# Kernel tuning notes

Hardware: AMD Instinct MI355X
Metric: run time of the kernel (lower is better)

The kernel has to match this reference:

```python
import jax, jax.numpy as jnp
import numpy as np

B, S, H, I = 2, 2048, 4096, 14336

def setup_inputs() -> dict:
    key = jax.random.key(0)
    k1, k2, k3, k4 = jax.random.split(key, 4)
    sH = 1.0 / np.sqrt(H)
    sI = 1.0 / np.sqrt(I)
    return {
        "x": jax.random.normal(k1, (B, S, H), dtype=jnp.float32),
        "w_gate": jax.random.normal(k2, (I, H), dtype=jnp.float32) * sH,
        "w_up": jax.random.normal(k3, (I, H), dtype=jnp.float32) * sH,
        "w_down": jax.random.normal(k4, (H, I), dtype=jnp.float32) * sI,
    }

def reference(x, w_gate, w_up, w_down):
    # SwiGLU gated MLP: down( silu(x @ Wg^T) * (x @ Wu^T) )
    g = jnp.einsum("bsh,ih->bsi", x, w_gate)   # [B,S,I]
    u = jnp.einsum("bsh,ih->bsi", x, w_up)     # [B,S,I]
    a = jax.nn.silu(g) * u                      # fused silu_mul
    d = jnp.einsum("bsi,hi->bsh", a, w_down)   # [B,S,H]
    return d
```

## Files before the change

kernel.cpp:

```cpp
#include <hip/hip_runtime.h>
#include <hip/hip_bf16.h>
#include <stdint.h>

typedef __bf16 bf16_t;
typedef __bf16 bf16x4 __attribute__((ext_vector_type(4)));
typedef __bf16 bf16x8 __attribute__((ext_vector_type(8)));
typedef float f32x4 __attribute__((ext_vector_type(4)));

#define LDS_CAST(p) ((__attribute__((address_space(3))) void*)(p))
#define GLB_CAST(p) ((const __attribute__((address_space(1))) void*)(p))

__device__ __forceinline__ void gl_lds16(const void* g, void* l) {
  __builtin_amdgcn_global_load_lds(GLB_CAST(g), LDS_CAST(l), 16, 0, 0);
}

#define MFMA16(a,b,c) __builtin_amdgcn_mfma_f32_16x16x32_bf16((a),(b),(c),0,0,0)
#define BARRIER() __builtin_amdgcn_s_barrier()
#define LGKM0()  asm volatile("s_waitcnt lgkmcnt(0)" ::: "memory")
#define PRIO(n)  __builtin_amdgcn_s_setprio(n)

template<int N> __device__ __forceinline__ void vmw() {
  if constexpr (N == 8)      asm volatile("s_waitcnt vmcnt(8)" ::: "memory");
  else if constexpr (N == 4) asm volatile("s_waitcnt vmcnt(4)" ::: "memory");
  else if constexpr (N == 0) asm volatile("s_waitcnt vmcnt(0)" ::: "memory");
}

static constexpr int M_TOT = 4096, H_DIM = 4096, I_DIM = 14336;

__global__ __launch_bounds__(256)
void k_conv(const float4* __restrict__ src, bf16x4* __restrict__ dst, long n4)
{
  long stride = (long)gridDim.x * blockDim.x;
  for (long i = (long)blockIdx.x * blockDim.x + threadIdx.x; i < n4; i += stride) {
    float4 v = src[i];
    bf16x4 o;
    o[0] = (bf16_t)v.x; o[1] = (bf16_t)v.y; o[2] = (bf16_t)v.z; o[3] = (bf16_t)v.w;
    dst[i] = o;
  }
}

__global__ __launch_bounds__(512, 2)
void k_gateup9(const bf16_t* __restrict__ X, const bf16_t* __restrict__ Wg,
               const bf16_t* __restrict__ Wu, bf16_t* __restrict__ Aout)
{
  __shared__ __align__(1024) char lds[131072];
  const int tid = threadIdx.x, wave = tid >> 6, lane = tid & 63;
  const int lr = lane & 15, kg = lane >> 4;
  const int xm = ((lr >> 3) & 1) << 5;
  const int wm = wave >> 2, wn = wave & 3;
  const int wb = wave * 1024;

  const int bid = blockIdx.x;
  const int bq  = bid >> 3;
  const int tn  = (bid & 7) * 14 + (bq >> 4);
  const int tm  = bq & 15;

  const int srow  = tid >> 2;
  const int scolb = ((tid & 3) * 16) ^ (((tid >> 5) & 1) << 5);

  const bf16_t* gX = X  + (size_t)(tm * 256 + srow) * H_DIM + (scolb >> 1);
  const bf16_t* gG = Wg + (size_t)(tn * 128 + srow) * H_DIM + (scolb >> 1);
  const bf16_t* gU = Wu + (size_t)(tn * 128 + srow) * H_DIM + (scolb >> 1);
  const size_t xh = (size_t)128 * H_DIM;

  const int ck   = (kg * 16) ^ xm;
  const int offA = (wm * 128 + lr) * 64 + ck;
  const int offG = 16384 + (wn * 32 + lr) * 64 + ck;
  const int offU = offG + 8192;

  const f32x4 vz = {0.f, 0.f, 0.f, 0.f};
  f32x4 accg[8][2], accu[8][2];
#pragma unroll
  for (int m = 0; m < 8; ++m)
#pragma unroll
    for (int n = 0; n < 2; ++n) { accg[m][n] = vz; accu[m][n] = vz; }

#define G1_STAGE(TT)                                                         \
  { char* sb = lds + (((TT) & 3) << 15) + wb;                                \
    const int kc = (TT) * 32;                                                \
    gl_lds16(gX + kc,      sb);                                              \
    gl_lds16(gX + xh + kc, sb + 8192);                                       \
    gl_lds16(gG + kc,      sb + 16384);                                      \
    gl_lds16(gU + kc,      sb + 24576); }

#define G1_READS(SET, TT)                                                    \
  { const char* rb = lds + (((TT) & 3) << 15);                               \
    _Pragma("unroll") for (int f = 0; f < 8; ++f)                            \
      a##SET[f] = *(const bf16x8*)(rb + offA + f * 1024);                    \
    _Pragma("unroll") for (int n = 0; n < 2; ++n) {                          \
      bg##SET[n] = *(const bf16x8*)(rb + offG + n * 1024);                   \
      bu##SET[n] = *(const bf16x8*)(rb + offU + n * 1024); } }

#define G1_MFMA(SET)                                                         \
  { PRIO(1);                                                                 \
    _Pragma("unroll") for (int m = 0; m < 8; ++m)                            \
    _Pragma("unroll") for (int n = 0; n < 2; ++n) {                          \
      accg[m][n] = MFMA16(a##SET[m], bg##SET[n], accg[m][n]);                \
      accu[m][n] = MFMA16(a##SET[m], bu##SET[n], accu[m][n]); }              \
    PRIO(0); }

  bf16x8 aA[8], bgA[2], buA[2];
  bf16x8 aB[8], bgB[2], buB[2];

  G1_STAGE(0); G1_STAGE(1); G1_STAGE(2);
  vmw<8>(); BARRIER();
  G1_READS(A, 0);

  const int NT = H_DIM / 32;
  for (int T = 0; T < NT - 4; T += 2) {
    vmw<4>(); BARRIER();
    G1_READS(B, T + 1);
    G1_STAGE(T + 3);
    G1_MFMA(A);
    vmw<4>(); BARRIER();
    G1_READS(A, T + 2);
    G1_STAGE(T + 4);
    G1_MFMA(B);
  }
  vmw<4>(); BARRIER(); G1_READS(B, NT - 3); G1_STAGE(NT - 1); G1_MFMA(A);
  vmw<4>(); BARRIER(); G1_READS(A, NT - 2);                   G1_MFMA(B);
  vmw<0>(); BARRIER(); G1_READS(B, NT - 1);                   G1_MFMA(A);
  G1_MFMA(B);
#undef G1_STAGE
#undef G1_READS
#undef G1_MFMA

  const int r0 = tm * 256 + wm * 128 + kg * 4;
  const int c0 = tn * 128 + wn * 32 + lr;
#pragma unroll
  for (int m = 0; m < 8; ++m)
#pragma unroll
    for (int n = 0; n < 2; ++n)
#pragma unroll
      for (int e = 0; e < 4; ++e) {
        float g = accg[m][n][e];
        float u = accu[m][n][e];
        float s = g / (1.0f + __expf(-g));
        Aout[(size_t)(r0 + m * 16 + e) * I_DIM + c0 + n * 16] = (bf16_t)(s * u);
      }
}

__global__ __launch_bounds__(512, 2)
void k_down10(const bf16_t* __restrict__ Aa, const bf16_t* __restrict__ Wd,
              float* __restrict__ D)
{
  __shared__ __align__(1024) char lds[131072];
  const int tid = threadIdx.x, wave = tid >> 6, lane = tid & 63;
  const int lr = lane & 15, kg = lane >> 4;
  const int xm = ((lr >> 3) & 1) << 5;
  const int wm = wave >> 2, wn = wave & 3;
  const int wb = wave * 1024;

  const int bid = blockIdx.x;
  const int bq  = bid >> 3;
  const int tn  = (bid & 7) * 2 + (bq >> 4);
  const int tm  = bq & 15;

  const int srow  = tid >> 2;
  const int scolb = ((tid & 3) * 16) ^ (((tid >> 5) & 1) << 5);

  const bf16_t* gA = Aa + (size_t)(tm * 256 + srow) * I_DIM + (scolb >> 1);
  const bf16_t* gB = Wd + (size_t)(tn * 256 + srow) * I_DIM + (scolb >> 1);
  const size_t hI = (size_t)128 * I_DIM;

  const int ck   = (kg * 16) ^ xm;
  const int offA = (wm * 128 + lr) * 64 + ck;
  const int offB = (wn * 64 + lr) * 64 + ck;

  const f32x4 vz = {0.f, 0.f, 0.f, 0.f};
  f32x4 acc[8][4];
#pragma unroll
  for (int m = 0; m < 8; ++m)
#pragma unroll
    for (int n = 0; n < 4; ++n) acc[m][n] = vz;

  gl_lds16(gA,           lds + 0     + wb);
  gl_lds16(gA + hI,      lds + 8192  + wb);
  gl_lds16(gB,           lds + 32768 + wb);
  gl_lds16(gB + hI,      lds + 40960 + wb);
  gl_lds16(gA + 32,      lds + 16384 + wb);
  gl_lds16(gA + hI + 32, lds + 24576 + wb);
  gl_lds16(gB + 32,      lds + 49152 + wb);
  gl_lds16(gB + hI + 32, lds + 57344 + wb);
  vmw<4>(); BARRIER();

  const int NT = I_DIM / 64;
  for (int T = 0; T <= NT - 2; ++T) {
    const char* bb = lds + (T & 1) * 65536;
    char* sb = lds + ((T + 1) & 1) * 65536 + wb;
    const bf16_t* gAn = gA + (T + 1) * 64;
    const bf16_t* gBn = gB + (T + 1) * 64;
    bf16x8 bv[4];
    {
      bf16x8 a[4];
#pragma unroll
      for (int f = 0; f < 4; ++f) a[f] = *(const bf16x8*)(bb + offA + f * 1024);
#pragma unroll
      for (int n = 0; n < 4; ++n) bv[n] = *(const bf16x8*)(bb + 32768 + offB + n * 1024);
      gl_lds16(gAn, sb); gl_lds16(gAn + hI, sb + 8192);
      BARRIER(); LGKM0();
      PRIO(1);
#pragma unroll
      for (int m = 0; m < 4; ++m)
#pragma unroll
        for (int n = 0; n < 4; ++n) acc[m][n] = MFMA16(a[m], bv[n], acc[m][n]);
      PRIO(0);
      BARRIER();
    }
    {
      bf16x8 a[4];
#pragma unroll
      for (int f = 0; f < 4; ++f) a[f] = *(const bf16x8*)(bb + offA + (f + 4) * 1024);
      gl_lds16(gBn, sb + 32768); gl_lds16(gBn + hI, sb + 40960);
      BARRIER(); LGKM0();
      PRIO(1);
#pragma unroll
      for (int m = 0; m < 4; ++m)
#pragma unroll
        for (int n = 0; n < 4; ++n) acc[4 + m][n] = MFMA16(a[m], bv[n], acc[4 + m][n]);
      PRIO(0);
      vmw<4>(); BARRIER();
    }
    {
      bf16x8 a[4];
#pragma unroll
      for (int f = 0; f < 4; ++f) a[f] = *(const bf16x8*)(bb + 16384 + offA + f * 1024);
#pragma unroll
      for (int n = 0; n < 4; ++n) bv[n] = *(const bf16x8*)(bb + 49152 + offB + n * 1024);
      gl_lds16(gAn + 32, sb + 16384); gl_lds16(gAn + hI + 32, sb + 24576);
      BARRIER(); LGKM0();
      PRIO(1);
#pragma unroll
      for (int m = 0; m < 4; ++m)
#pragma unroll
        for (int n = 0; n < 4; ++n) acc[m][n] = MFMA16(a[m], bv[n], acc[m][n]);
      PRIO(0);
      BARRIER();
    }
    {
      bf16x8 a[4];
#pragma unroll
      for (int f = 0; f < 4; ++f) a[f] = *(const bf16x8*)(bb + 16384 + offA + (f + 4) * 1024);
      gl_lds16(gBn + 32, sb + 49152); gl_lds16(gBn + hI + 32, sb + 57344);
      BARRIER(); LGKM0();
      PRIO(1);
#pragma unroll
      for (int m = 0; m < 4; ++m)
#pragma unroll
        for (int n = 0; n < 4; ++n) acc[4 + m][n] = MFMA16(a[m], bv[n], acc[4 + m][n]);
      PRIO(0);
      vmw<4>(); BARRIER();
    }
  }
  {
    const char* bb = lds + ((NT - 1) & 1) * 65536;
    bf16x8 bv[4];
    { bf16x8 a[4];
#pragma unroll
      for (int f = 0; f < 4; ++f) a[f] = *(const bf16x8*)(bb + offA + f * 1024);
#pragma unroll
      for (int n = 0; n < 4; ++n) bv[n] = *(const bf16x8*)(bb + 32768 + offB + n * 1024);
      BARRIER(); LGKM0(); PRIO(1);
#pragma unroll
      for (int m = 0; m < 4; ++m)
#pragma unroll
        for (int n = 0; n < 4; ++n) acc[m][n] = MFMA16(a[m], bv[n], acc[m][n]);
      PRIO(0); BARRIER(); }
    { bf16x8 a[4];
#pragma unroll
      for (int f = 0; f < 4; ++f) a[f] = *(const bf16x8*)(bb + offA + (f + 4) * 1024);
      BARRIER(); LGKM0(); PRIO(1);
#pragma unroll
      for (int m = 0; m < 4; ++m)
#pragma unroll
        for (int n = 0; n < 4; ++n) acc[4 + m][n] = MFMA16(a[m], bv[n], acc[4 + m][n]);
      PRIO(0); vmw<0>(); BARRIER(); }
    { bf16x8 a[4];
#pragma unroll
      for (int f = 0; f < 4; ++f) a[f] = *(const bf16x8*)(bb + 16384 + offA + f * 1024);
#pragma unroll
      for (int n = 0; n < 4; ++n) bv[n] = *(const bf16x8*)(bb + 49152 + offB + n * 1024);
      LGKM0(); PRIO(1);
#pragma unroll
      for (int m = 0; m < 4; ++m)
#pragma unroll
        for (int n = 0; n < 4; ++n) acc[m][n] = MFMA16(a[m], bv[n], acc[m][n]);
      PRIO(0); }
    { bf16x8 a[4];
#pragma unroll
      for (int f = 0; f < 4; ++f) a[f] = *(const bf16x8*)(bb + 16384 + offA + (f + 4) * 1024);
      LGKM0(); PRIO(1);
#pragma unroll
      for (int m = 0; m < 4; ++m)
#pragma unroll
        for (int n = 0; n < 4; ++n) acc[4 + m][n] = MFMA16(a[m], bv[n], acc[4 + m][n]);
      PRIO(0); }
  }

  const int r0 = tm * 256 + wm * 128 + kg * 4;
  const int c0 = tn * 256 + wn * 64 + lr;
#pragma unroll
  for (int m = 0; m < 8; ++m)
#pragma unroll
    for (int n = 0; n < 4; ++n)
#pragma unroll
      for (int e = 0; e < 4; ++e)
        D[(size_t)(r0 + m * 16 + e) * H_DIM + c0 + n * 16] = acc[m][n][e];
}

extern "C" void kernel_launch(void* const* d_in, const int* in_sizes, int n_in,
                              void* d_out, int out_size, void* d_ws, size_t ws_size,
                              hipStream_t stream) {
  const float* x  = (const float*)d_in[0];
  const float* wg = (const float*)d_in[1];
  const float* wu = (const float*)d_in[2];
  const float* wd = (const float*)d_in[3];
  float* out = (float*)d_out;

  const size_t A_BYTES = (size_t)M_TOT * I_DIM * 2;
  const size_t X_BYTES = (size_t)M_TOT * H_DIM * 2;
  const size_t W_BYTES = (size_t)I_DIM * H_DIM * 2;
  char* ws = (char*)d_ws;
  bf16_t* Ab  = (bf16_t*)(ws);
  bf16_t* Xb  = (bf16_t*)(ws + A_BYTES);
  bf16_t* Wgb = (bf16_t*)(ws + A_BYTES + X_BYTES);
  bf16_t* Wub = (bf16_t*)(ws + A_BYTES + X_BYTES + W_BYTES);
  bf16_t* Wdb = Wgb;

  const long nX = (long)M_TOT * H_DIM / 4;
  const long nW = (long)I_DIM * H_DIM / 4;

  k_conv<<<dim3(2048), dim3(256), 0, stream>>>((const float4*)x,  (bf16x4*)Xb,  nX);
  k_conv<<<dim3(2048), dim3(256), 0, stream>>>((const float4*)wg, (bf16x4*)Wgb, nW);
  k_conv<<<dim3(2048), dim3(256), 0, stream>>>((const float4*)wu, (bf16x4*)Wub, nW);

  k_gateup9<<<dim3(16 * 112), dim3(512), 0, stream>>>(Xb, Wgb, Wub, Ab);

  k_conv<<<dim3(2048), dim3(256), 0, stream>>>((const float4*)wd, (bf16x4*)Wdb, nW);

  k_down10<<<dim3(16 * 16), dim3(512), 0, stream>>>(Ab, Wdb, out);
}
```

Before: 1.436 ms.

## Fuse w_down fp32-to-bf16 conversion into down-projection GEMM staging

The down-projection kernel now reads fp32 w_down directly from global memory into registers, converts to bf16 and writes to LDS, removing the separate w_down conversion pass and its round trip through memory. The three remaining conversion launches are merged into one kernel. The B-tile pipeline changes from async global-to-LDS loads spread across four phases to register loads issued at the start of each tile with a full vmcnt(0) wait before the LDS write, and the peeled tail is folded into the loop. The fp32 weight tile is reread by each of the 16 M-tile blocks, doubling B-operand traffic, and the register staging adds VGPR pressure and exposed latency.

```diff
diff --git a/kernel.cpp b/kernel.cpp
--- a/kernel.cpp
+++ b/kernel.cpp
@@ -28,14 +28,27 @@
 static constexpr int M_TOT = 4096, H_DIM = 4096, I_DIM = 14336;
 
 __global__ __launch_bounds__(256)
-void k_conv(const float4* __restrict__ src, bf16x4* __restrict__ dst, long n4)
+void k_conv3(const float4* __restrict__ x,  const float4* __restrict__ wg,
+             const float4* __restrict__ wu, bf16x4* __restrict__ Xb,
+             bf16x4* __restrict__ Wgb, bf16x4* __restrict__ Wub,
+             long nX, long nW)
 {
-  long stride = (long)gridDim.x * blockDim.x;
-  for (long i = (long)blockIdx.x * blockDim.x + threadIdx.x; i < n4; i += stride) {
-    float4 v = src[i];
-    bf16x4 o;
+  const long stride = (long)gridDim.x * blockDim.x;
+  const long t0 = (long)blockIdx.x * blockDim.x + threadIdx.x;
+  for (long i = t0; i < nX; i += stride) {
+    float4 v = x[i]; bf16x4 o;
     o[0] = (bf16_t)v.x; o[1] = (bf16_t)v.y; o[2] = (bf16_t)v.z; o[3] = (bf16_t)v.w;
-    dst[i] = o;
+    Xb[i] = o;
+  }
+  for (long i = t0; i < nW; i += stride) {
+    float4 v = wg[i]; bf16x4 o;
+    o[0] = (bf16_t)v.x; o[1] = (bf16_t)v.y; o[2] = (bf16_t)v.z; o[3] = (bf16_t)v.w;
+    Wgb[i] = o;
+  }
+  for (long i = t0; i < nW; i += stride) {
+    float4 v = wu[i]; bf16x4 o;
+    o[0] = (bf16_t)v.x; o[1] = (bf16_t)v.y; o[2] = (bf16_t)v.z; o[3] = (bf16_t)v.w;
+    Wub[i] = o;
   }
 }
 
@@ -141,7 +154,7 @@
 }
 
 __global__ __launch_bounds__(512, 2)
-void k_down10(const bf16_t* __restrict__ Aa, const bf16_t* __restrict__ Wd,
+void k_down11(const bf16_t* __restrict__ Aa, const float* __restrict__ Wf,
               float* __restrict__ D)
 {
   __shared__ __align__(1024) char lds[131072];
@@ -158,9 +171,10 @@
 
   const int srow  = tid >> 2;
   const int scolb = ((tid & 3) * 16) ^ (((tid >> 5) & 1) << 5);
-
-  const bf16_t* gA = Aa + (size_t)(tm * 256 + srow) * I_DIM + (scolb >> 1);
-  const bf16_t* gB = Wd + (size_t)(tn * 256 + srow) * I_DIM + (scolb >> 1);
+  const int scol8 = scolb >> 1;
+
+  const bf16_t* gA = Aa + (size_t)(tm * 256 + srow) * I_DIM + scol8;
+  const float*  fB = Wf + (size_t)(tn * 256 + srow) * I_DIM + scol8;
   const size_t hI = (size_t)128 * I_DIM;
 
   const int ck   = (kg * 16) ^ xm;
@@ -174,22 +188,60 @@
 #pragma unroll
     for (int n = 0; n < 4; ++n) acc[m][n] = vz;
 
-  gl_lds16(gA,           lds + 0     + wb);
-  gl_lds16(gA + hI,      lds + 8192  + wb);
-  gl_lds16(gB,           lds + 32768 + wb);
-  gl_lds16(gB + hI,      lds + 40960 + wb);
-  gl_lds16(gA + 32,      lds + 16384 + wb);
-  gl_lds16(gA + hI + 32, lds + 24576 + wb);
-  gl_lds16(gB + 32,      lds + 49152 + wb);
-  gl_lds16(gB + hI + 32, lds + 57344 + wb);
-  vmw<4>(); BARRIER();
+  const int dst0 = 32768 + tid * 16;
+  const int dst1 = 40960 + tid * 16;
+  const int dst2 = 49152 + tid * 16;
+  const int dst3 = 57344 + tid * 16;
+
+#define B_LOAD(kc)                                                           \
+    float4 v0 = *(const float4*)(fB + (kc));                                 \
+    float4 v1 = *(const float4*)(fB + (kc) + 4);                             \
+    float4 v2 = *(const float4*)(fB + hI + (kc));                            \
+    float4 v3 = *(const float4*)(fB + hI + (kc) + 4);                        \
+    float4 v4 = *(const float4*)(fB + (kc) + 32);                            \
+    float4 v5 = *(const float4*)(fB + (kc) + 36);                            \
+    float4 v6 = *(const float4*)(fB + hI + (kc) + 32);                       \
+    float4 v7 = *(const float4*)(fB + hI + (kc) + 36);
+
+#define B_CVT_WRITE(sb)                                                      \
+    { bf16x8 w;                                                              \
+      w[0]=(bf16_t)v0.x; w[1]=(bf16_t)v0.y; w[2]=(bf16_t)v0.z;               \
+      w[3]=(bf16_t)v0.w; w[4]=(bf16_t)v1.x; w[5]=(bf16_t)v1.y;               \
+      w[6]=(bf16_t)v1.z; w[7]=(bf16_t)v1.w;                                  \
+      *(bf16x8*)((sb) + dst0) = w;                                           \
+      w[0]=(bf16_t)v2.x; w[1]=(bf16_t)v2.y; w[2]=(bf16_t)v2.z;               \
+      w[3]=(bf16_t)v2.w; w[4]=(bf16_t)v3.x; w[5]=(bf16_t)v3.y;               \
+      w[6]=(bf16_t)v3.z; w[7]=(bf16_t)v3.w;                                  \
+      *(bf16x8*)((sb) + dst1) = w;                                           \
+      w[0]=(bf16_t)v4.x; w[1]=(bf16_t)v4.y; w[2]=(bf16_t)v4.z;               \
+      w[3]=(bf16_t)v4.w; w[4]=(bf16_t)v5.x; w[5]=(bf16_t)v5.y;               \
+      w[6]=(bf16_t)v5.z; w[7]=(bf16_t)v5.w;                                  \
+      *(bf16x8*)((sb) + dst2) = w;                                           \
+      w[0]=(bf16_t)v6.x; w[1]=(bf16_t)v6.y; w[2]=(bf16_t)v6.z;               \
+      w[3]=(bf16_t)v6.w; w[4]=(bf16_t)v7.x; w[5]=(bf16_t)v7.y;               \
+      w[6]=(bf16_t)v7.z; w[7]=(bf16_t)v7.w;                                  \
+      *(bf16x8*)((sb) + dst3) = w; }
+
+  {
+    char* sb = lds;
+    gl_lds16(gA,          sb + 0     + wb);
+    gl_lds16(gA + hI,     sb + 8192  + wb);
+    gl_lds16(gA + 32,     sb + 16384 + wb);
+    gl_lds16(gA + hI + 32,sb + 24576 + wb);
+    B_LOAD(0);
+    vmw<0>();
+    B_CVT_WRITE(sb);
+    LGKM0();
+  }
+  BARRIER();
 
   const int NT = I_DIM / 64;
-  for (int T = 0; T <= NT - 2; ++T) {
+  for (int T = 0; T < NT; ++T) {
     const char* bb = lds + (T & 1) * 65536;
-    char* sb = lds + ((T + 1) & 1) * 65536 + wb;
-    const bf16_t* gAn = gA + (T + 1) * 64;
-    const bf16_t* gBn = gB + (T + 1) * 64;
+    char* sb = lds + ((T + 1) & 1) * 65536;
+    const bool stg = (T < NT - 1);
+    const int kc = (T + 1) * 64;
+    float4 v0, v1, v2, v3, v4, v5, v6, v7;
     bf16x8 bv[4];
     {
       bf16x8 a[4];
@@ -197,7 +249,20 @@
       for (int f = 0; f < 4; ++f) a[f] = *(const bf16x8*)(bb + offA + f * 1024);
 #pragma unroll
       for (int n = 0; n < 4; ++n) bv[n] = *(const bf16x8*)(bb + 32768 + offB + n * 1024);
-      gl_lds16(gAn, sb); gl_lds16(gAn + hI, sb + 8192);
+      if (stg) {
+        gl_lds16(gA + kc,           sb + 0     + wb);
+        gl_lds16(gA + hI + kc,      sb + 8192  + wb);
+        gl_lds16(gA + kc + 32,      sb + 16384 + wb);
+        gl_lds16(gA + hI + kc + 32, sb + 24576 + wb);
+        v0 = *(const float4*)(fB + kc);
+        v1 = *(const float4*)(fB + kc + 4);
+        v2 = *(const float4*)(fB + hI + kc);
+        v3 = *(const float4*)(fB + hI + kc + 4);
+        v4 = *(const float4*)(fB + kc + 32);
+        v5 = *(const float4*)(fB + kc + 36);
+        v6 = *(const float4*)(fB + hI + kc + 32);
+        v7 = *(const float4*)(fB + hI + kc + 36);
+      }
       BARRIER(); LGKM0();
       PRIO(1);
 #pragma unroll
@@ -211,7 +276,6 @@
       bf16x8 a[4];
 #pragma unroll
       for (int f = 0; f < 4; ++f) a[f] = *(const bf16x8*)(bb + offA + (f + 4) * 1024);
-      gl_lds16(gBn, sb + 32768); gl_lds16(gBn + hI, sb + 40960);
       BARRIER(); LGKM0();
       PRIO(1);
 #pragma unroll
@@ -219,7 +283,7 @@
 #pragma unroll
         for (int n = 0; n < 4; ++n) acc[4 + m][n] = MFMA16(a[m], bv[n], acc[4 + m][n]);
       PRIO(0);
-      vmw<4>(); BARRIER();
+      BARRIER();
     }
     {
       bf16x8 a[4];
@@ -227,7 +291,6 @@
       for (int f = 0; f < 4; ++f) a[f] = *(const bf16x8*)(bb + 16384 + offA + f * 1024);
 #pragma unroll
       for (int n = 0; n < 4; ++n) bv[n] = *(const bf16x8*)(bb + 49152 + offB + n * 1024);
-      gl_lds16(gAn + 32, sb + 16384); gl_lds16(gAn + hI + 32, sb + 24576);
       BARRIER(); LGKM0();
       PRIO(1);
 #pragma unroll
@@ -241,7 +304,6 @@
       bf16x8 a[4];
 #pragma unroll
       for (int f = 0; f < 4; ++f) a[f] = *(const bf16x8*)(bb + 16384 + offA + (f + 4) * 1024);
-      gl_lds16(gBn + 32, sb + 49152); gl_lds16(gBn + hI + 32, sb + 57344);
       BARRIER(); LGKM0();
       PRIO(1);
 #pragma unroll
@@ -249,53 +311,14 @@
 #pragma unroll
         for (int n = 0; n < 4; ++n) acc[4 + m][n] = MFMA16(a[m], bv[n], acc[4 + m][n]);
       PRIO(0);
-      vmw<4>(); BARRIER();
+      vmw<0>();
+      if (stg) { B_CVT_WRITE(sb); }
+      LGKM0();
+      BARRIER();
     }
   }
-  {
-    const char* bb = lds + ((NT - 1) & 1) * 65536;
-    bf16x8 bv[4];
-    { bf16x8 a[4];
-#pragma unroll
-      for (int f = 0; f < 4; ++f) a[f] = *(const bf16x8*)(bb + offA + f * 1024);
-#pragma unroll
-      for (int n = 0; n < 4; ++n) bv[n] = *(const bf16x8*)(bb + 32768 + offB + n * 1024);
-      BARRIER(); LGKM0(); PRIO(1);
-#pragma unroll
-      for (int m = 0; m < 4; ++m)
-#pragma unroll
-        for (int n = 0; n < 4; ++n) acc[m][n] = MFMA16(a[m], bv[n], acc[m][n]);
-      PRIO(0); BARRIER(); }
-    { bf16x8 a[4];
-#pragma unroll
-      for (int f = 0; f < 4; ++f) a[f] = *(const bf16x8*)(bb + offA + (f + 4) * 1024);
-      BARRIER(); LGKM0(); PRIO(1);
-#pragma unroll
-      for (int m = 0; m < 4; ++m)
-#pragma unroll
-        for (int n = 0; n < 4; ++n) acc[4 + m][n] = MFMA16(a[m], bv[n], acc[4 + m][n]);
-      PRIO(0); vmw<0>(); BARRIER(); }
-    { bf16x8 a[4];
-#pragma unroll
-      for (int f = 0; f < 4; ++f) a[f] = *(const bf16x8*)(bb + 16384 + offA + f * 1024);
-#pragma unroll
-      for (int n = 0; n < 4; ++n) bv[n] = *(const bf16x8*)(bb + 49152 + offB + n * 1024);
-      LGKM0(); PRIO(1);
-#pragma unroll
-      for (int m = 0; m < 4; ++m)
-#pragma unroll
-        for (int n = 0; n < 4; ++n) acc[m][n] = MFMA16(a[m], bv[n], acc[m][n]);
-      PRIO(0); }
-    { bf16x8 a[4];
-#pragma unroll
-      for (int f = 0; f < 4; ++f) a[f] = *(const bf16x8*)(bb + 16384 + offA + (f + 4) * 1024);
-      LGKM0(); PRIO(1);
-#pragma unroll
-      for (int m = 0; m < 4; ++m)
-#pragma unroll
-        for (int n = 0; n < 4; ++n) acc[4 + m][n] = MFMA16(a[m], bv[n], acc[4 + m][n]);
-      PRIO(0); }
-  }
+#undef B_LOAD
+#undef B_CVT_WRITE
 
   const int r0 = tm * 256 + wm * 128 + kg * 4;
   const int c0 = tn * 256 + wn * 64 + lr;
@@ -325,18 +348,15 @@
   bf16_t* Xb  = (bf16_t*)(ws + A_BYTES);
   bf16_t* Wgb = (bf16_t*)(ws + A_BYTES + X_BYTES);
   bf16_t* Wub = (bf16_t*)(ws + A_BYTES + X_BYTES + W_BYTES);
-  bf16_t* Wdb = Wgb;
 
   const long nX = (long)M_TOT * H_DIM / 4;
   const long nW = (long)I_DIM * H_DIM / 4;
 
-  k_conv<<<dim3(2048), dim3(256), 0, stream>>>((const float4*)x,  (bf16x4*)Xb,  nX);
-  k_conv<<<dim3(2048), dim3(256), 0, stream>>>((const float4*)wg, (bf16x4*)Wgb, nW);
-  k_conv<<<dim3(2048), dim3(256), 0, stream>>>((const float4*)wu, (bf16x4*)Wub, nW);
+  k_conv3<<<dim3(2048), dim3(256), 0, stream>>>(
+      (const float4*)x, (const float4*)wg, (const float4*)wu,
+      (bf16x4*)Xb, (bf16x4*)Wgb, (bf16x4*)Wub, nX, nW);
 
   k_gateup9<<<dim3(16 * 112), dim3(512), 0, stream>>>(Xb, Wgb, Wub, Ab);
 
-  k_conv<<<dim3(2048), dim3(256), 0, stream>>>((const float4*)wd, (bf16x4*)Wdb, nW);
-
-  k_down10<<<dim3(16 * 16), dim3(512), 0, stream>>>(Ab, Wdb, out);
-}
+  k_down11<<<dim3(16 * 16), dim3(512), 0, stream>>>(Ab, wd, out);
+}
```

Measured after the change: 1.730 ms. 1.2x slower.
